# Kernel optimization log

Measured on AMD Instinct MI355X. Metric: run time of the kernel, lower is better.

## Reference

```python
import jax, jax.numpy as jnp
import numpy as np

N_EMBED = 1024
HIDDEN = 2752  # find_multiple(int(8/3*1024), 32)
NUM_EXPERTS = 8
TOP_K = 2
AUX_COEFF = 0.01


def _swiglu(x, wg, wu, wd):
    # x: [N,C]; wg,wu: [H,C]; wd: [C,H]  (nn.Linear weight layout, y = x @ W.T)
    return (jax.nn.silu(x @ wg.T) * (x @ wu.T)) @ wd.T


def setup_inputs() -> dict:
    key = jax.random.key(0)
    ks = jax.random.split(key, 8)
    s = 0.02
    return {
        "x": jax.random.normal(ks[0], (2, 2048, N_EMBED), dtype=jnp.float32),
        "gate_w": jax.random.normal(ks[1], (NUM_EXPERTS, N_EMBED), dtype=jnp.float32) * s,
        "expert_gate_w": jax.random.normal(ks[2], (NUM_EXPERTS, HIDDEN, N_EMBED), dtype=jnp.float32) * s,
        "expert_up_w": jax.random.normal(ks[3], (NUM_EXPERTS, HIDDEN, N_EMBED), dtype=jnp.float32) * s,
        "expert_down_w": jax.random.normal(ks[4], (NUM_EXPERTS, N_EMBED, HIDDEN), dtype=jnp.float32) * s,
        "shared_gate_w": jax.random.normal(ks[5], (HIDDEN, N_EMBED), dtype=jnp.float32) * s,
        "shared_up_w": jax.random.normal(ks[6], (HIDDEN, N_EMBED), dtype=jnp.float32) * s,
        "shared_down_w": jax.random.normal(ks[7], (N_EMBED, HIDDEN), dtype=jnp.float32) * s,
    }


def reference(x, gate_w, expert_gate_w, expert_up_w, expert_down_w,
              shared_gate_w, shared_up_w, shared_down_w):
    B, T, C = x.shape
    xf = x.reshape(-1, C)                      # [N, C]
    N = xf.shape[0]

    # shared expert (always-on)
    shared_out = _swiglu(xf, shared_gate_w, shared_up_w, shared_down_w)

    # gating
    logits = xf @ gate_w.T                     # [N, E]
    top_w, top_i = jax.lax.top_k(logits, TOP_K)
    top_w = jax.nn.softmax(top_w.astype(jnp.float32), axis=-1)  # [N, K]

    # load-balancing aux loss
    mask = jax.nn.one_hot(top_i, NUM_EXPERTS, dtype=jnp.float32).sum(axis=1)  # [N, E]
    frac_selected = mask.mean(axis=0)
    mean_probs = jax.nn.softmax(logits.astype(jnp.float32), axis=-1).mean(axis=0)
    aux_loss = AUX_COEFF * (frac_selected * mean_probs).sum()

    # dense per-token per-expert combine weights (0 for unselected experts)
    w_dense = jnp.zeros((N, NUM_EXPERTS), jnp.float32)
    w_dense = w_dense.at[jnp.arange(N)[:, None], top_i].add(top_w)  # [N, E]

    routed = jnp.zeros_like(xf)
    for e in range(NUM_EXPERTS):
        routed = routed + _swiglu(xf, expert_gate_w[e], expert_up_w[e],
                                  expert_down_w[e]) * w_dense[:, e:e + 1]

    final = (shared_out + routed).reshape(B, T, C)
    return final, aux_loss
```

## Files before the change

### kernel.cpp

```cpp
#include <hip/hip_runtime.h>
#include <hip/hip_bf16.h>
#include <math.h>

#define N_TOK 4096
#define CDIM 1024
#define HDIM 2752
#define NEXP 8

typedef __bf16 bf16_t;
typedef __bf16 bf16x8 __attribute__((ext_vector_type(8)));
typedef float f32x4 __attribute__((ext_vector_type(4)));

__device__ __forceinline__ void gload_lds16(const void* g, void* l) {
  __builtin_amdgcn_global_load_lds(
      (const __attribute__((address_space(1))) unsigned int*)g,
      (__attribute__((address_space(3))) unsigned int*)l, 16, 0, 0);
}

struct CastG {
  const float* src[6];
  bf16_t* dst[6];
  int start[7];
  const float* x;
  const float* gw;
  int* top_i; float* top_w; float* probs_tok; bf16_t* xb;
};
__global__ void moe_cast_gate(CastG c) {
  const int b = blockIdx.x;
  if (b < c.start[6]) {
    int k = 0;
#pragma unroll
    for (int i = 0; i < 5; ++i) k += (b >= c.start[i + 1]);
    size_t i4 = (size_t)(b - c.start[k]) * 256 + threadIdx.x;
    float4 v = ((const float4*)c.src[k])[i4];
    union { bf16_t b4[4]; unsigned long long u; } pk;
    pk.b4[0] = (bf16_t)v.x; pk.b4[1] = (bf16_t)v.y;
    pk.b4[2] = (bf16_t)v.z; pk.b4[3] = (bf16_t)v.w;
    ((unsigned long long*)c.dst[k])[i4] = pk.u;
    return;
  }
  const int gb = b - c.start[6];
  const int wid = threadIdx.x >> 6, lane = threadIdx.x & 63;
  const int n = gb * 4 + wid;
  const float* xr = c.x + (size_t)n * CDIM;
  float xv[16];
  for (int j = 0; j < 16; j += 4)
    *(float4*)&xv[j] = *(const float4*)(xr + lane * 16 + j);
  {
    union { bf16_t bb[4]; unsigned long long u; } pk;
    unsigned long long* dst = (unsigned long long*)(c.xb + (size_t)n * CDIM + lane * 16);
    for (int j = 0; j < 16; j += 4) {
      pk.bb[0] = (bf16_t)xv[j]; pk.bb[1] = (bf16_t)xv[j+1];
      pk.bb[2] = (bf16_t)xv[j+2]; pk.bb[3] = (bf16_t)xv[j+3];
      dst[j >> 2] = pk.u;
    }
  }
  double part[NEXP];
  for (int e = 0; e < NEXP; ++e) {
    const float* gr = c.gw + e * CDIM + lane * 16;
    double s = 0.0;
    for (int j = 0; j < 16; j += 4) {
      float4 g = *(const float4*)(gr + j);
      s += (double)xv[j] * g.x + (double)xv[j+1] * g.y + (double)xv[j+2] * g.z + (double)xv[j+3] * g.w;
    }
    part[e] = s;
  }
  for (int off = 32; off; off >>= 1)
    for (int e = 0; e < NEXP; ++e) part[e] += __shfl_xor(part[e], off);
  if (lane == 0) {
    int i0 = 0; double l0 = part[0];
    for (int e = 1; e < NEXP; ++e) if (part[e] > l0) { l0 = part[e]; i0 = e; }
    int i1 = -1; double l1 = -1e300;
    for (int e = 0; e < NEXP; ++e) if (e != i0 && part[e] > l1) { l1 = part[e]; i1 = e; }
    double ed = exp(l1 - l0);
    float w0 = (float)(1.0 / (1.0 + ed));
    float w1 = (float)(ed / (1.0 + ed));
    c.top_i[2*n] = i0; c.top_i[2*n+1] = i1;
    c.top_w[2*n] = w0; c.top_w[2*n+1] = w1;
    double Z = 0.0, pe[NEXP];
    for (int e = 0; e < NEXP; ++e) { pe[e] = exp(part[e] - l0); Z += pe[e]; }
    for (int e = 0; e < NEXP; ++e) c.probs_tok[(size_t)n * NEXP + e] = (float)(pe[e] / Z);
  }
}

__global__ __launch_bounds__(256) void moe_reduce16(
    const float* __restrict__ probs_tok, const int* __restrict__ top_i,
    int* __restrict__ pcnt, float* __restrict__ psum) {
  const int b = blockIdx.x, t = threadIdx.x;
  const int wid = t >> 6, lane = t & 63;
  const int n = b * 256 + t;
  const int e0 = top_i[2*n], e1 = top_i[2*n + 1];
  float4 p0 = ((const float4*)(probs_tok + (size_t)n * NEXP))[0];
  float4 p1 = ((const float4*)(probs_tok + (size_t)n * NEXP))[1];
  float pv[8] = {p0.x, p0.y, p0.z, p0.w, p1.x, p1.y, p1.z, p1.w};
  __shared__ int lc[4][NEXP];
  __shared__ float ls[4][NEXP];
  for (int e = 0; e < NEXP; ++e) {
    int c = (e0 == e) + (e1 == e);
    float s = pv[e];
    for (int o = 32; o; o >>= 1) { c += __shfl_xor(c, o); s += __shfl_xor(s, o); }
    if (lane == 0) { lc[wid][e] = c; ls[wid][e] = s; }
  }
  __syncthreads();
  if (t < NEXP) {
    pcnt[b * NEXP + t] = lc[0][t] + lc[1][t] + lc[2][t] + lc[3][t];
    psum[b * NEXP + t] = ls[0][t] + ls[1][t] + ls[2][t] + ls[3][t];
  }
}

__global__ __launch_bounds__(256) void moe_scatter16(
    const int* __restrict__ top_i, const float* __restrict__ top_w,
    const int* __restrict__ pcnt, const float* __restrict__ psum,
    int* __restrict__ cnts_g, int* __restrict__ offs_g,
    int* __restrict__ rowlist, float* __restrict__ wlist,
    float* __restrict__ out_aux) {
  const int b = blockIdx.x, t = threadIdx.x;
  const int wid = t >> 6, lane = t & 63;
  __shared__ int tot_s[NEXP], pre_s[NEXP], offs_s[NEXP];
  __shared__ int wc[4][NEXP];
  if (t < NEXP) {
    int e = t, tot = 0, pre = 0;
    for (int bb = 0; bb < 16; ++bb) {
      int v = pcnt[bb * NEXP + e];
      pre += (bb < b) ? v : 0;
      tot += v;
    }
    tot_s[e] = tot; pre_s[e] = pre;
  }
  __syncthreads();
  if (t == 0) {
    int o = 0;
    for (int e = 0; e < NEXP; ++e) { offs_s[e] = o; o += tot_s[e]; }
    if (b == 0) {
      double aux = 0.0;
      for (int e = 0; e < NEXP; ++e) {
        float ps = 0.f;
        for (int bb = 0; bb < 16; ++bb) ps += psum[bb * NEXP + e];
        aux += (double)tot_s[e] * (double)ps;
        cnts_g[e] = tot_s[e]; offs_g[e] = offs_s[e];
      }
      out_aux[0] = (float)(0.01 * aux / ((double)N_TOK * (double)N_TOK));
    }
  }
  __syncthreads();
  const int n = b * 256 + t;
  const int e0 = top_i[2*n], e1 = top_i[2*n + 1];
  const float w0 = top_w[2*n], w1 = top_w[2*n + 1];
  for (int e = 0; e < NEXP; ++e) {
    unsigned long long m0 = __ballot(e0 == e);
    unsigned long long m1 = __ballot(e1 == e);
    if (lane == 0) wc[wid][e] = __popcll(m0) + __popcll(m1);
  }
  __syncthreads();
  const unsigned long long lt = ((unsigned long long)1 << lane) - 1;
  for (int e = 0; e < NEXP; ++e) {
    unsigned long long m0 = __ballot(e0 == e);
    unsigned long long m1 = __ballot(e1 == e);
    int wp = 0;
    for (int w = 0; w < wid; ++w) wp += wc[w][e];
    int base = offs_s[e] + pre_s[e] + wp;
    if (e0 == e) {
      int p = base + __popcll(m0 & lt);
      rowlist[p] = n; wlist[p] = w0;
    }
    if (e1 == e) {
      int p = base + __popcll(m0) + __popcll(m1 & lt);
      rowlist[p] = n; wlist[p] = w1;
    }
  }
}

__launch_bounds__(256)
__global__ void moe_gu(const bf16_t* __restrict__ xb,
                       const bf16_t* __restrict__ Wg_r, const bf16_t* __restrict__ Wu_r,
                       const bf16_t* __restrict__ Wg_s, const bf16_t* __restrict__ Wu_s,
                       bf16_t* __restrict__ hout,
                       const int* __restrict__ rowlist, const int* __restrict__ offs,
                       const int* __restrict__ cnts) {
  const int z = blockIdx.z;
  const bool routed = z < NEXP;
  int cnt, hbase, loff = 0;
  const bf16_t *Wg, *Wu;
  if (routed) {
    cnt = cnts[z]; loff = offs[z]; hbase = loff;
    if ((int)blockIdx.y * 128 >= cnt) return;
    Wg = Wg_r + (size_t)z * HDIM * CDIM;
    Wu = Wu_r + (size_t)z * HDIM * CDIM;
  } else {
    cnt = N_TOK; hbase = 2 * N_TOK;
    Wg = Wg_s; Wu = Wu_s;
  }
  const int m0 = blockIdx.y * 128, n0 = blockIdx.x * 64;

  __shared__ alignas(16) bf16_t lA[128 * 64];
  __shared__ alignas(16) bf16_t lB[128 * 64];

  const int tid = threadIdx.x, wid = tid >> 6, lane = tid & 63;
  const int r8 = lane >> 3, c8 = lane & 7;
  const int fr = lane & 15, hi = lane >> 4;

  const bf16_t* gA[4];
  for (int i = 0; i < 4; ++i) {
    int r = wid * 32 + i * 8 + r8;
    int tok;
    if (routed) { int mm = m0 + r < cnt ? m0 + r : cnt - 1; tok = rowlist[loff + mm]; }
    else tok = m0 + r;
    gA[i] = xb + (size_t)tok * CDIM + c8 * 8;
  }
  const bf16_t* gB[4];
  for (int i = 0; i < 4; ++i) {
    int br = wid * 32 + i * 8 + r8;
    gB[i] = (br < 64 ? Wg + (size_t)(n0 + br) * CDIM
                     : Wu + (size_t)(n0 + br - 64) * CDIM) + c8 * 8;
  }

  f32x4 accG[2][4] = {}; f32x4 accU[2][4] = {};

  for (int kt = 0; kt < CDIM / 64; ++kt) {
    if (kt) __syncthreads();
    for (int i = 0; i < 4; ++i) gload_lds16(gA[i] + kt * 64, lA + (wid * 32 + i * 8) * 64);
    for (int i = 0; i < 4; ++i) gload_lds16(gB[i] + kt * 64, lB + (wid * 32 + i * 8) * 64);
    __syncthreads();
    for (int kk = 0; kk < 2; ++kk) {
      const int kb = kk * 32 + hi * 8;
      bf16x8 a[2], bg[4], bu[4];
      for (int i = 0; i < 2; ++i) a[i] = *(const bf16x8*)(lA + (wid * 32 + i * 16 + fr) * 64 + kb);
      for (int j = 0; j < 4; ++j) {
        bg[j] = *(const bf16x8*)(lB + (j * 16 + fr) * 64 + kb);
        bu[j] = *(const bf16x8*)(lB + (64 + j * 16 + fr) * 64 + kb);
      }
      for (int i = 0; i < 2; ++i)
        for (int j = 0; j < 4; ++j) {
          accG[i][j] = __builtin_amdgcn_mfma_f32_16x16x32_bf16(a[i], bg[j], accG[i][j], 0, 0, 0);
          accU[i][j] = __builtin_amdgcn_mfma_f32_16x16x32_bf16(a[i], bu[j], accU[i][j], 0, 0, 0);
        }
    }
  }
  for (int i = 0; i < 2; ++i)
    for (int j = 0; j < 4; ++j)
      for (int r = 0; r < 4; ++r) {
        int lm = wid * 32 + i * 16 + hi * 4 + r;
        if (routed && m0 + lm >= cnt) continue;
        float g = accG[i][j][r], u = accU[i][j][r];
        float hv = (g / (1.f + __expf(-g))) * u;
        hout[(size_t)(hbase + m0 + lm) * HDIM + n0 + j * 16 + fr] = (bf16_t)hv;
      }
}

__launch_bounds__(256)
__global__ void moe_down(const bf16_t* __restrict__ hin, const bf16_t* __restrict__ Wd_r,
                         const bf16_t* __restrict__ Wd_s,
                         float* __restrict__ outp,
                         const float* __restrict__ wlist, const int* __restrict__ rowlist,
                         const int* __restrict__ offs, const int* __restrict__ cnts) {
  const int z = blockIdx.z;
  const bool routed = z < NEXP;
  int cnt, hbase;
  const bf16_t* Wd;
  if (routed) {
    cnt = cnts[z]; hbase = offs[z];
    if ((int)blockIdx.y * 128 >= cnt) return;
    Wd = Wd_r + (size_t)z * CDIM * HDIM;
  } else {
    cnt = N_TOK; hbase = 2 * N_TOK;
    Wd = Wd_s;
  }
  const int m0 = blockIdx.y * 128, n0 = blockIdx.x * 128;

  __shared__ alignas(16) bf16_t lA[128 * 64];
  __shared__ alignas(16) bf16_t lB[128 * 64];

  const int tid = threadIdx.x, wid = tid >> 6, lane = tid & 63;
  const int wm = wid >> 1, wn = wid & 1;
  const int r8 = lane >> 3, c8 = lane & 7;
  const int fr = lane & 15, hi = lane >> 4;

  const bf16_t* gA[4];
  for (int i = 0; i < 4; ++i) {
    int r = wid * 32 + i * 8 + r8;
    int mm = (routed && m0 + r >= cnt) ? cnt - 1 : m0 + r;
    gA[i] = hin + (size_t)(hbase + mm) * HDIM + c8 * 8;
  }
  const bf16_t* gB[4];
  for (int i = 0; i < 4; ++i) {
    int br = wid * 32 + i * 8 + r8;
    gB[i] = Wd + (size_t)(n0 + br) * HDIM + c8 * 8;
  }

  f32x4 acc[4][4] = {};

  for (int kt = 0; kt < HDIM / 64; ++kt) {
    if (kt) __syncthreads();
    for (int i = 0; i < 4; ++i) gload_lds16(gA[i] + kt * 64, lA + (wid * 32 + i * 8) * 64);
    for (int i = 0; i < 4; ++i) gload_lds16(gB[i] + kt * 64, lB + (wid * 32 + i * 8) * 64);
    __syncthreads();
    for (int kk = 0; kk < 2; ++kk) {
      const int kb = kk * 32 + hi * 8;
      bf16x8 a[4], b[4];
      for (int i = 0; i < 4; ++i) a[i] = *(const bf16x8*)(lA + (wm * 64 + i * 16 + fr) * 64 + kb);
      for (int j = 0; j < 4; ++j) b[j] = *(const bf16x8*)(lB + (wn * 64 + j * 16 + fr) * 64 + kb);
      for (int i = 0; i < 4; ++i)
        for (int j = 0; j < 4; ++j)
          acc[i][j] = __builtin_amdgcn_mfma_f32_16x16x32_bf16(a[i], b[j], acc[i][j], 0, 0, 0);
    }
  }
  for (int i = 0; i < 4; ++i)
    for (int j = 0; j < 4; ++j)
      for (int r = 0; r < 4; ++r) {
        int lm = wm * 64 + i * 16 + hi * 4 + r;
        if (routed && m0 + lm >= cnt) continue;
        float v = acc[i][j][r];
        int col = n0 + wn * 64 + j * 16 + fr;
        if (routed) {
          int pos = hbase + m0 + lm;
          int tok = rowlist[pos];
          atomicAdd(&outp[(size_t)tok * CDIM + col], v * wlist[pos]);
        } else {
          atomicAdd(&outp[(size_t)(m0 + lm) * CDIM + col], v);
        }
      }
}

extern "C" void kernel_launch(void* const* d_in, const int* in_sizes, int n_in,
                              void* d_out, int out_size, void* d_ws, size_t ws_size,
                              hipStream_t stream) {
  const float* x   = (const float*)d_in[0];
  const float* gw  = (const float*)d_in[1];
  const float* egw = (const float*)d_in[2];
  const float* euw = (const float*)d_in[3];
  const float* edw = (const float*)d_in[4];
  const float* sgw = (const float*)d_in[5];
  const float* suw = (const float*)d_in[6];
  const float* sdw = (const float*)d_in[7];
  float* out = (float*)d_out;

  char* ws = (char*)d_ws;
  size_t off = 0;
  auto alloc = [&](size_t bytes) -> void* {
    void* p = ws + off; off = (off + bytes + 255) & ~(size_t)255; return p;
  };
  const size_t EW = (size_t)NEXP * HDIM * CDIM;
  const size_t SW = (size_t)HDIM * CDIM;
  bf16_t* xb    = (bf16_t*)alloc((size_t)N_TOK * CDIM * 2);
  bf16_t* egw_b = (bf16_t*)alloc(EW * 2);
  bf16_t* euw_b = (bf16_t*)alloc(EW * 2);
  bf16_t* edw_b = (bf16_t*)alloc(EW * 2);
  bf16_t* sgw_b = (bf16_t*)alloc(SW * 2);
  bf16_t* suw_b = (bf16_t*)alloc(SW * 2);
  bf16_t* sdw_b = (bf16_t*)alloc(SW * 2);
  bf16_t* h     = (bf16_t*)alloc((size_t)(3 * N_TOK + 256) * HDIM * 2);
  int*    ctrl  = (int*)alloc(256);
  int* cnts = ctrl; int* offs = ctrl + 8;
  int*   top_i    = (int*)alloc((size_t)N_TOK * 2 * 4);
  float* top_w    = (float*)alloc((size_t)N_TOK * 2 * 4);
  int*   rowlist  = (int*)alloc((size_t)2 * N_TOK * 4);
  float* wlist    = (float*)alloc((size_t)2 * N_TOK * 4);
  float* probs_tok = (float*)alloc((size_t)N_TOK * NEXP * 4);
  int*   pcnt     = (int*)alloc(16 * NEXP * 4);
  float* psum     = (float*)alloc(16 * NEXP * 4);

  hipMemsetAsync(out, 0, (size_t)N_TOK * CDIM * 4, stream);

  CastG cg;
  cg.src[0] = egw; cg.dst[0] = egw_b;
  cg.src[1] = euw; cg.dst[1] = euw_b;
  cg.src[2] = edw; cg.dst[2] = edw_b;
  cg.src[3] = sgw; cg.dst[3] = sgw_b;
  cg.src[4] = suw; cg.dst[4] = suw_b;
  cg.src[5] = sdw; cg.dst[5] = sdw_b;
  int ew_blk = (int)(EW / 1024), sw_blk = (int)(SW / 1024);
  cg.start[0] = 0;
  cg.start[1] = ew_blk;     cg.start[2] = 2 * ew_blk; cg.start[3] = 3 * ew_blk;
  cg.start[4] = 3 * ew_blk + sw_blk;
  cg.start[5] = 3 * ew_blk + 2 * sw_blk;
  cg.start[6] = 3 * ew_blk + 3 * sw_blk;
  cg.x = x; cg.gw = gw;
  cg.top_i = top_i; cg.top_w = top_w; cg.probs_tok = probs_tok; cg.xb = xb;
  moe_cast_gate<<<cg.start[6] + N_TOK / 4, 256, 0, stream>>>(cg);

  moe_reduce16<<<16, 256, 0, stream>>>(probs_tok, top_i, pcnt, psum);
  moe_scatter16<<<16, 256, 0, stream>>>(top_i, top_w, pcnt, psum, cnts, offs,
                                        rowlist, wlist, out + (size_t)N_TOK * CDIM);

  moe_gu<<<dim3(HDIM / 64, N_TOK / 128, NEXP + 1), 256, 0, stream>>>(
      xb, egw_b, euw_b, sgw_b, suw_b, h, rowlist, offs, cnts);
  moe_down<<<dim3(CDIM / 128, N_TOK / 128, NEXP + 1), 256, 0, stream>>>(
      h, edw_b, sdw_b, out, wlist, rowlist, offs, cnts);
}
```

Before: 487.0 us.

## Replace down-projection atomics with per-pair buffer plus combine kernel; XCD swizzle

The down-projection kernel no longer atomically accumulates into the output. Routed experts write weighted results to a per-pair scratch buffer, and the shared expert writes the output directly. A new combine kernel then adds the two routed pair results per token using positions recorded during scatter, which also removes the output memset. The down grid is flattened to one dimension with an XCD-aware block remap for better L2 locality, at the cost of an extra 32MB write and read of scratch traffic.

New measurement: 488.3 us. No clear change (+0.3%).

```diff
diff --git a/kernel.cpp b/kernel.cpp
--- a/kernel.cpp
+++ b/kernel.cpp
@@ -15,6 +15,12 @@
   __builtin_amdgcn_global_load_lds(
       (const __attribute__((address_space(1))) unsigned int*)g,
       (__attribute__((address_space(3))) unsigned int*)l, 16, 0, 0);
+}
+
+__device__ __forceinline__ int xcd_swz(int orig, int nwg) {
+  int q = nwg >> 3, r = nwg & 7;
+  int xcd = orig & 7, lin = orig >> 3;
+  return (xcd < r ? xcd * (q + 1) : r * (q + 1) + (xcd - r) * q) + lin;
 }
 
 struct CastG {
@@ -113,7 +119,7 @@
     const int* __restrict__ pcnt, const float* __restrict__ psum,
     int* __restrict__ cnts_g, int* __restrict__ offs_g,
     int* __restrict__ rowlist, float* __restrict__ wlist,
-    float* __restrict__ out_aux) {
+    int* __restrict__ pair_pos, float* __restrict__ out_aux) {
   const int b = blockIdx.x, t = threadIdx.x;
   const int wid = t >> 6, lane = t & 63;
   __shared__ int tot_s[NEXP], pre_s[NEXP], offs_s[NEXP];
@@ -161,11 +167,11 @@
     int base = offs_s[e] + pre_s[e] + wp;
     if (e0 == e) {
       int p = base + __popcll(m0 & lt);
-      rowlist[p] = n; wlist[p] = w0;
+      rowlist[p] = n; wlist[p] = w0; pair_pos[2*n] = p;
     }
     if (e1 == e) {
       int p = base + __popcll(m0) + __popcll(m1 & lt);
-      rowlist[p] = n; wlist[p] = w1;
+      rowlist[p] = n; wlist[p] = w1; pair_pos[2*n + 1] = p;
     }
   }
 }
@@ -250,22 +256,24 @@
 __launch_bounds__(256)
 __global__ void moe_down(const bf16_t* __restrict__ hin, const bf16_t* __restrict__ Wd_r,
                          const bf16_t* __restrict__ Wd_s,
-                         float* __restrict__ outp,
-                         const float* __restrict__ wlist, const int* __restrict__ rowlist,
+                         float* __restrict__ outp, float* __restrict__ eo,
+                         const float* __restrict__ wlist,
                          const int* __restrict__ offs, const int* __restrict__ cnts) {
   const int z = blockIdx.z;
   const bool routed = z < NEXP;
+  const int wg = xcd_swz(blockIdx.x, (CDIM / 128) * (N_TOK / 128));
+  const int ym = wg & 31, xn = wg >> 5;
   int cnt, hbase;
   const bf16_t* Wd;
   if (routed) {
     cnt = cnts[z]; hbase = offs[z];
-    if ((int)blockIdx.y * 128 >= cnt) return;
+    if (ym * 128 >= cnt) return;
     Wd = Wd_r + (size_t)z * CDIM * HDIM;
   } else {
     cnt = N_TOK; hbase = 2 * N_TOK;
     Wd = Wd_s;
   }
-  const int m0 = blockIdx.y * 128, n0 = blockIdx.x * 128;
+  const int m0 = ym * 128, n0 = xn * 128;
 
   __shared__ alignas(16) bf16_t lA[128 * 64];
   __shared__ alignas(16) bf16_t lB[128 * 64];
@@ -313,12 +321,27 @@
         int col = n0 + wn * 64 + j * 16 + fr;
         if (routed) {
           int pos = hbase + m0 + lm;
-          int tok = rowlist[pos];
-          atomicAdd(&outp[(size_t)tok * CDIM + col], v * wlist[pos]);
+          eo[(size_t)pos * CDIM + col] = v * wlist[pos];
         } else {
-          atomicAdd(&outp[(size_t)(m0 + lm) * CDIM + col], v);
+          outp[(size_t)(m0 + lm) * CDIM + col] = v;
         }
       }
+}
+
+__global__ void moe_combine(float* __restrict__ outp, const float* __restrict__ eo,
+                            const int* __restrict__ pair_pos) {
+  size_t i4 = (size_t)blockIdx.x * 256 + threadIdx.x;
+  int n = (int)(i4 >> 8);
+  int c4 = (int)(i4 & 255);
+  int p0 = pair_pos[2*n], p1 = pair_pos[2*n + 1];
+  const float4* eo4 = (const float4*)eo;
+  float4 a = ((const float4*)outp)[i4];
+  float4 b = eo4[(size_t)p0 * 256 + c4];
+  float4 c = eo4[(size_t)p1 * 256 + c4];
+  float4 r;
+  r.x = a.x + b.x + c.x; r.y = a.y + b.y + c.y;
+  r.z = a.z + b.z + c.z; r.w = a.w + b.w + c.w;
+  ((float4*)outp)[i4] = r;
 }
 
 extern "C" void kernel_launch(void* const* d_in, const int* in_sizes, int n_in,
@@ -349,17 +372,17 @@
   bf16_t* suw_b = (bf16_t*)alloc(SW * 2);
   bf16_t* sdw_b = (bf16_t*)alloc(SW * 2);
   bf16_t* h     = (bf16_t*)alloc((size_t)(3 * N_TOK + 256) * HDIM * 2);
+  float*  eo    = (float*)alloc((size_t)2 * N_TOK * CDIM * 4);
   int*    ctrl  = (int*)alloc(256);
   int* cnts = ctrl; int* offs = ctrl + 8;
   int*   top_i    = (int*)alloc((size_t)N_TOK * 2 * 4);
   float* top_w    = (float*)alloc((size_t)N_TOK * 2 * 4);
+  int*   pair_pos = (int*)alloc((size_t)N_TOK * 2 * 4);
   int*   rowlist  = (int*)alloc((size_t)2 * N_TOK * 4);
   float* wlist    = (float*)alloc((size_t)2 * N_TOK * 4);
   float* probs_tok = (float*)alloc((size_t)N_TOK * NEXP * 4);
   int*   pcnt     = (int*)alloc(16 * NEXP * 4);
   float* psum     = (float*)alloc(16 * NEXP * 4);
-
-  hipMemsetAsync(out, 0, (size_t)N_TOK * CDIM * 4, stream);
 
   CastG cg;
   cg.src[0] = egw; cg.dst[0] = egw_b;
@@ -380,10 +403,12 @@
 
   moe_reduce16<<<16, 256, 0, stream>>>(probs_tok, top_i, pcnt, psum);
   moe_scatter16<<<16, 256, 0, stream>>>(top_i, top_w, pcnt, psum, cnts, offs,
-                                        rowlist, wlist, out + (size_t)N_TOK * CDIM);
+                                        rowlist, wlist, pair_pos,
+                                        out + (size_t)N_TOK * CDIM);
 
   moe_gu<<<dim3(HDIM / 64, N_TOK / 128, NEXP + 1), 256, 0, stream>>>(
       xb, egw_b, euw_b, sgw_b, suw_b, h, rowlist, offs, cnts);
-  moe_down<<<dim3(CDIM / 128, N_TOK / 128, NEXP + 1), 256, 0, stream>>>(
-      h, edw_b, sdw_b, out, wlist, rowlist, offs, cnts);
-}
+  moe_down<<<dim3((CDIM / 128) * (N_TOK / 128), 1, NEXP + 1), 256, 0, stream>>>(
+      h, edw_b, sdw_b, out, eo, wlist, offs, cnts);
+  moe_combine<<<4096, 256, 0, stream>>>(out, eo, pair_pos);
+}
```
